# Kernel optimization log

Measured on AMD Instinct MI355X. Metric: run time of the kernel, lower is better.

Reference implementation:

```python
import jax, jax.numpy as jnp
import numpy as np

HEADS = 8
NEG_SLOPE = 0.2  # PyG GATConv default LeakyReLU slope


def _gat_layer(x, src, dst, W, a_src, a_dst, bias, heads, out_ch):
    """PyG-style GATConv (concat heads, self-loops already appended, eval mode).
    x: [N, F_in]; src/dst: [E_tot] int; W: [F_in, heads*out_ch];
    a_src/a_dst: [heads, out_ch]; bias: [heads*out_ch].
    """
    N = x.shape[0]
    h = (x @ W).reshape(N, heads, out_ch)                      # [N, H, C]
    # per-node attention logits (gathered per edge as scalars, not features)
    al_s = jnp.einsum('nhc,hc->nh', h, a_src)                  # [N, H]
    al_d = jnp.einsum('nhc,hc->nh', h, a_dst)                  # [N, H]
    e = jax.nn.leaky_relu(al_s[src] + al_d[dst], negative_slope=NEG_SLOPE)  # [E, H]
    # segment softmax over incoming edges of each target node (stable)
    e_max = jax.ops.segment_max(e, dst, num_segments=N)        # self-loops => no empty segments
    ex = jnp.exp(e - e_max[dst])
    denom = jax.ops.segment_sum(ex, dst, num_segments=N)
    alpha = ex / (denom[dst] + 1e-16)                          # [E, H]
    # gather source features, weight, scatter-add to targets
    out = jax.ops.segment_sum(h[src] * alpha[:, :, None], dst, num_segments=N)  # [N, H, C]
    return out.reshape(N, heads * out_ch) + bias


def setup_inputs() -> dict:
    key = jax.random.key(0)
    ks = jax.random.split(key, 16)
    N, E, F_IN, NUM_CLASSES = 50000, 1600000, 128, 16
    s = 0.1
    return {
        'x': jax.random.normal(ks[0], (N, F_IN), dtype=jnp.float32),
        'edge_index': jax.random.randint(ks[1], (2, E), 0, N, dtype=jnp.int64),
        # GAT layer 1: 128 -> 8 heads x 8
        'W1': jax.random.normal(ks[2], (F_IN, 64), dtype=jnp.float32) * s,
        'a1_src': jax.random.normal(ks[3], (8, 8), dtype=jnp.float32) * s,
        'a1_dst': jax.random.normal(ks[4], (8, 8), dtype=jnp.float32) * s,
        'b1': jnp.zeros((64,), dtype=jnp.float32),
        # GAT layer 2: 64 -> 8 heads x 4
        'W2': jax.random.normal(ks[5], (64, 32), dtype=jnp.float32) * s,
        'a2_src': jax.random.normal(ks[6], (8, 4), dtype=jnp.float32) * s,
        'a2_dst': jax.random.normal(ks[7], (8, 4), dtype=jnp.float32) * s,
        'b2': jnp.zeros((32,), dtype=jnp.float32),
        # torch MultiheadAttention(32, 8): packed in_proj [96,32], out_proj [32,32]
        'in_proj_w': jax.random.normal(ks[8], (96, 32), dtype=jnp.float32) * s,
        'in_proj_b': jnp.zeros((96,), dtype=jnp.float32),
        'out_proj_w': jax.random.normal(ks[9], (32, 32), dtype=jnp.float32) * s,
        'out_proj_b': jnp.zeros((32,), dtype=jnp.float32),
        # fc: 32 -> num_classes
        'fc_w': jax.random.normal(ks[10], (NUM_CLASSES, 32), dtype=jnp.float32) * s,
        'fc_b': jnp.zeros((NUM_CLASSES,), dtype=jnp.float32),
    }


def reference(x, edge_index, W1, a1_src, a1_dst, b1, W2, a2_src, a2_dst, b2,
              in_proj_w, in_proj_b, out_proj_w, out_proj_b, fc_w, fc_b):
    N = x.shape[0]
    loops = jnp.arange(N, dtype=edge_index.dtype)
    src = jnp.concatenate([edge_index[0], loops])  # PyG add_self_loops=True
    dst = jnp.concatenate([edge_index[1], loops])

    h = jax.nn.elu(_gat_layer(x, src, dst, W1, a1_src, a1_dst, b1, HEADS, 8))   # [N, 64]
    h = jax.nn.elu(_gat_layer(h, src, dst, W2, a2_src, a2_dst, b2, HEADS, 4))   # [N, 32]

    # MultiheadAttention on h.unsqueeze(0): shape [1, N, 32] with torch's
    # seq-first layout => seq_len = 1, batch = N. Softmax over a single key
    # is identically 1 for every head, so out = out_proj(v_proj(h)).
    v = h @ in_proj_w[64:96].T + in_proj_b[64:96]   # v-projection slice of packed in_proj
    h = v @ out_proj_w.T + out_proj_b               # [N, 32]

    logits = h @ fc_w.T + fc_b                      # [N, num_classes]
    return jax.nn.log_softmax(logits, axis=1)
```

## Files before the change

### kernel.cpp

```cpp
#include <hip/hip_runtime.h>
#include <hip/hip_bf16.h>
#include <math.h>


#define BSHIFT 7
#define BMASK  ((1 << BSHIFT) - 1)
#define MAXNB  512
#define TILE   8192
#define XST    136

typedef __attribute__((ext_vector_type(8))) short short8;
typedef __attribute__((ext_vector_type(4))) float floatx4;
typedef __attribute__((ext_vector_type(2))) float floatx2;

__device__ __forceinline__ unsigned short f2bf(float f) {
    union { float f; unsigned int u; } v; v.f = f;
    unsigned int u = v.u;
    return (unsigned short)((u + 0x7FFFu + ((u >> 16) & 1u)) >> 16);
}
__device__ __forceinline__ float lrelu(float e) { return fmaxf(e, 0.2f * e); }
__device__ __forceinline__ float elu(float o) {
    return (o > 0.f) ? o : (__expf(o) - 1.f);
}

__global__ __launch_bounds__(256) void bin_scatter1_kernel(
    const int* __restrict__ ei, int E, int Et, int NB, int CAP,
    int* __restrict__ gcount, unsigned int* __restrict__ rec) {
    __shared__ unsigned int lrec[TILE];
    __shared__ int h[MAXNB];
    __shared__ int cur[MAXNB];
    int t = threadIdx.x;
    for (int i = t; i < NB; i += 256) h[i] = 0;
    int tile0 = blockIdx.x * TILE;
    int cnt = Et - tile0; if (cnt > TILE) cnt = TILE;
    __syncthreads();
    for (int j = t; j < cnt; j += 256) {
        int jj = tile0 + j;
        int srcv, d;
        if (jj < E) { srcv = ei[jj]; d = ei[E + jj]; } else { srcv = jj - E; d = jj - E; }
        lrec[j] = (unsigned)srcv | ((unsigned)d << 16);
        atomicAdd(&h[d >> BSHIFT], 1);
    }
    __syncthreads();
    for (int i = t; i < NB; i += 256)
        cur[i] = h[i] ? atomicAdd(&gcount[i], h[i]) : 0;
    __syncthreads();
    for (int j = t; j < cnt; j += 256) {
        unsigned v = lrec[j];
        int b = v >> (16 + BSHIFT);
        int pos = atomicAdd(&cur[b], 1);
        if (pos < CAP)
            rec[(size_t)b * CAP + pos] =
                (v & 0xFFFFu) | ((((v >> 16) & BMASK)) << 16);
    }
}

__global__ __launch_bounds__(512) void scan_fold_kernel(
    const int* __restrict__ gcount, int* __restrict__ bbase, int NB, int CAP,
    const float* __restrict__ in_proj_w, const float* __restrict__ in_proj_b,
    const float* __restrict__ out_proj_w, const float* __restrict__ out_proj_b,
    const float* __restrict__ fc_w, const float* __restrict__ fc_b,
    float* __restrict__ M, float* __restrict__ bf) {
    __shared__ int s[512];
    __shared__ float Wvo[32 * 32];
    __shared__ float bvo[32];
    int t = threadIdx.x;
    if (blockIdx.x == 0) {
        int v = 0;
        if (t < NB) { v = gcount[t]; if (v > CAP) v = CAP; }
        s[t] = v;
        __syncthreads();
        for (int off = 1; off < 512; off <<= 1) {
            int u = (t >= off) ? s[t - off] : 0;
            __syncthreads();
            s[t] += u;
            __syncthreads();
        }
        if (t < NB) bbase[t] = s[t] - v;
    } else {
        const float* Wv = in_proj_w + 64 * 32;
        const float* bv = in_proj_b + 64;
        for (int idx = t; idx < 1024; idx += 512) {
            int i = idx >> 5, j = idx & 31;
            float acc = 0.f;
            for (int k = 0; k < 32; ++k) acc += out_proj_w[i * 32 + k] * Wv[k * 32 + j];
            Wvo[idx] = acc;
        }
        if (t < 32) {
            float acc = 0.f;
            for (int k = 0; k < 32; ++k) acc += out_proj_w[t * 32 + k] * bv[k];
            bvo[t] = acc + out_proj_b[t];
        }
        __syncthreads();
        for (int idx = t; idx < 16 * 32; idx += 512) {
            int cc = idx >> 5, j = idx & 31;
            float acc = 0.f;
            for (int i = 0; i < 32; ++i) acc += fc_w[cc * 32 + i] * Wvo[i * 32 + j];
            M[idx] = acc;
        }
        if (t < 16) {
            float acc = 0.f;
            for (int i = 0; i < 32; ++i) acc += fc_w[t * 32 + i] * bvo[i];
            bf[t] = acc + fc_b[t];
        }
    }
}

__global__ __launch_bounds__(256) void csr_finalize_kernel(
    const unsigned int* __restrict__ rec, const int* __restrict__ gcount,
    const int* __restrict__ bbase, int* __restrict__ rowp,
    unsigned short* __restrict__ esrc, int N, int Et, int CAP) {
    __shared__ int h[128];
    __shared__ int nb[128];
    __shared__ int cur[128];
    int b = blockIdx.x, t = threadIdx.x;
    size_t rbase = (size_t)b * CAP;
    int cnt = gcount[b]; if (cnt > CAP) cnt = CAP;
    int obase = bbase[b];
    if (t < 128) h[t] = 0;
    __syncthreads();
    for (int i = t; i < cnt; i += 256)
        atomicAdd(&h[(rec[rbase + i] >> 16) & 127], 1);
    __syncthreads();
    if (t == 0) {
        int run = obase;
        for (int i = 0; i < 128; ++i) { nb[i] = run; run += h[i]; }
    }
    __syncthreads();
    if (t < 128) cur[t] = nb[t];
    int n0 = b << BSHIFT;
    if (t < 128 && n0 + t < N) rowp[n0 + t] = nb[t];
    if (b == 0 && t == 0) rowp[N] = Et;
    __syncthreads();
    for (int i = t; i < cnt; i += 256) {
        unsigned r = rec[rbase + i];
        int pos = atomicAdd(&cur[(r >> 16) & 127], 1);
        esrc[pos] = (unsigned short)(r & 0xFFFFu);
    }
}

__global__ __launch_bounds__(256) void gemm1_mfma_kernel(
    const float* __restrict__ x, const float* __restrict__ W,
    const float* __restrict__ a_src, const float* __restrict__ a_dst,
    unsigned int* __restrict__ h1p, float* __restrict__ als,
    float* __restrict__ ald, int N) {
    __shared__ __align__(16) unsigned short xs[64 * XST];
    __shared__ __align__(16) unsigned short wt[64 * XST];
    int t = threadIdx.x;
    int nb = blockIdx.x * 64;
#pragma unroll
    for (int r = 0; r < 8; ++r) {
        int p = t + 256 * r;
        int row = p >> 5;
        int c4  = p & 31;
        int n = nb + row;
        float4 v = (n < N) ? ((const float4*)x)[(size_t)n * 32 + c4]
                           : make_float4(0.f, 0.f, 0.f, 0.f);
        unsigned short* dst = &xs[row * XST + c4 * 4];
        dst[0] = f2bf(v.x); dst[1] = f2bf(v.y);
        dst[2] = f2bf(v.z); dst[3] = f2bf(v.w);
    }
    {
        int n = t & 63, kg = t >> 6;
#pragma unroll
        for (int c = 0; c < 4; ++c) {
            int k0 = kg * 32 + c * 8;
            unsigned short* dst = &wt[n * XST + k0];
#pragma unroll
            for (int j = 0; j < 8; ++j)
                dst[j] = f2bf(W[(k0 + j) * 64 + n]);
        }
    }
    __syncthreads();
    int wave = t >> 6, lane = t & 63;
    int m16 = lane & 15, quad = lane >> 4;
    floatx4 acc[4];
#pragma unroll
    for (int i = 0; i < 4; ++i) acc[i] = (floatx4){0.f, 0.f, 0.f, 0.f};
#pragma unroll
    for (int k = 0; k < 4; ++k) {
        int koff = k * 32 + quad * 8;
        short8 afrag = *(const short8*)&xs[(wave * 16 + m16) * XST + koff];
#pragma unroll
        for (int nt = 0; nt < 4; ++nt) {
            short8 bfrag = *(const short8*)&wt[(nt * 16 + m16) * XST + koff];
            acc[nt] = __builtin_amdgcn_mfma_f32_16x16x32_bf16(afrag, bfrag, acc[nt], 0, 0, 0);
        }
    }
    __syncthreads();
    float* hs = (float*)xs;
#pragma unroll
    for (int nt = 0; nt < 4; ++nt)
#pragma unroll
        for (int r = 0; r < 4; ++r)
            hs[(wave * 16 + quad * 4 + r) * 65 + nt * 16 + m16] = acc[nt][r];
    __syncthreads();
    float asv = a_src[lane], adv = a_dst[lane];
    for (int itn = 0; itn < 16; ++itn) {
        int nl = wave * 16 + itn;
        int n = nb + nl;
        if (n >= N) break;
        float v = hs[nl * 65 + lane];
        float ps = v * asv, pd = v * adv;
        ps += __shfl_xor(ps, 1); ps += __shfl_xor(ps, 2); ps += __shfl_xor(ps, 4);
        pd += __shfl_xor(pd, 1); pd += __shfl_xor(pd, 2); pd += __shfl_xor(pd, 4);
        if ((lane & 7) == 0) {
            als[n * 8 + (lane >> 3)] = ps;
            ald[n * 8 + (lane >> 3)] = pd;
        }
        if (lane < 16) {
            const float* hr = &hs[nl * 65 + lane * 4];
            int pk = __builtin_amdgcn_cvt_pk_fp8_f32(hr[0], hr[1], 0, false);
            pk = __builtin_amdgcn_cvt_pk_fp8_f32(hr[2], hr[3], pk, true);
            h1p[(size_t)n * 16 + lane] = (unsigned)pk;
        }
    }
}

__global__ __launch_bounds__(256) void gat_agg64_g2_kernel(
    const int* __restrict__ rowp, const unsigned short* __restrict__ esrc,
    const unsigned int* __restrict__ feat, const float* __restrict__ als,
    const float* __restrict__ ald_arr, const float* __restrict__ bias,
    const float* __restrict__ W2, const float* __restrict__ a2s,
    const float* __restrict__ a2d,
    char* __restrict__ rec2, float* __restrict__ ald2, int N) {
    __shared__ __align__(16) float W2p[2][8][32][4];
    __shared__ __align__(16) float oL[4][64];
    __shared__ __align__(16) float h2L[4][32];
    int t = threadIdx.x;
    for (int idx = t; idx < 2048; idx += 256) {
        int k = idx >> 5, l = idx & 31;
        W2p[k >> 5][(k & 31) >> 2][l][k & 3] = W2[idx];
    }
    __syncthreads();
    const int lane = t & 63;
    const int wv = t >> 6;
    const int e = lane >> 4;
    const int c = lane & 15;
    const int hd = c >> 1;
    int n = blockIdx.x * 4 + wv;
    if (n >= N) return;
    float aldv = ald_arr[n * 8 + hd];
    int beg = rowp[n], end = rowp[n + 1];
    float dA = 0.f, dB = 0.f;
    floatx2 p0a = {0.f, 0.f}, p0b = {0.f, 0.f};
    floatx2 p1a = {0.f, 0.f}, p1b = {0.f, 0.f};
    floatx2 p2a = {0.f, 0.f}, p2b = {0.f, 0.f};
    floatx2 p3a = {0.f, 0.f}, p3b = {0.f, 0.f};
    int i = beg;
    for (; i + 32 <= end; i += 32) {
        int s0 = esrc[i + e],      s1 = esrc[i + 4 + e];
        int s2 = esrc[i + 8 + e],  s3 = esrc[i + 12 + e];
        int s4 = esrc[i + 16 + e], s5 = esrc[i + 20 + e];
        int s6 = esrc[i + 24 + e], s7 = esrc[i + 28 + e];
        float e0 = als[s0 * 8 + hd], e1 = als[s1 * 8 + hd];
        float e2 = als[s2 * 8 + hd], e3 = als[s3 * 8 + hd];
        float e4 = als[s4 * 8 + hd], e5 = als[s5 * 8 + hd];
        float e6 = als[s6 * 8 + hd], e7 = als[s7 * 8 + hd];
        unsigned g0 = feat[s0 * 16 + c], g1 = feat[s1 * 16 + c];
        unsigned g2 = feat[s2 * 16 + c], g3 = feat[s3 * 16 + c];
        unsigned g4 = feat[s4 * 16 + c], g5 = feat[s5 * 16 + c];
        unsigned g6 = feat[s6 * 16 + c], g7 = feat[s7 * 16 + c];
        float w0 = __expf(lrelu(e0 + aldv));
        float w1 = __expf(lrelu(e1 + aldv));
        float w2 = __expf(lrelu(e2 + aldv));
        float w3 = __expf(lrelu(e3 + aldv));
        float w4 = __expf(lrelu(e4 + aldv));
        float w5 = __expf(lrelu(e5 + aldv));
        float w6 = __expf(lrelu(e6 + aldv));
        float w7 = __expf(lrelu(e7 + aldv));
        dA += w0 + w2; dB += w1 + w3;
        dA += w4 + w6; dB += w5 + w7;
        p0a += w0 * __builtin_amdgcn_cvt_pk_f32_fp8(g0, false);
        p0b += w0 * __builtin_amdgcn_cvt_pk_f32_fp8(g0, true);
        p1a += w1 * __builtin_amdgcn_cvt_pk_f32_fp8(g1, false);
        p1b += w1 * __builtin_amdgcn_cvt_pk_f32_fp8(g1, true);
        p2a += w2 * __builtin_amdgcn_cvt_pk_f32_fp8(g2, false);
        p2b += w2 * __builtin_amdgcn_cvt_pk_f32_fp8(g2, true);
        p3a += w3 * __builtin_amdgcn_cvt_pk_f32_fp8(g3, false);
        p3b += w3 * __builtin_amdgcn_cvt_pk_f32_fp8(g3, true);
        p0a += w4 * __builtin_amdgcn_cvt_pk_f32_fp8(g4, false);
        p0b += w4 * __builtin_amdgcn_cvt_pk_f32_fp8(g4, true);
        p1a += w5 * __builtin_amdgcn_cvt_pk_f32_fp8(g5, false);
        p1b += w5 * __builtin_amdgcn_cvt_pk_f32_fp8(g5, true);
        p2a += w6 * __builtin_amdgcn_cvt_pk_f32_fp8(g6, false);
        p2b += w6 * __builtin_amdgcn_cvt_pk_f32_fp8(g6, true);
        p3a += w7 * __builtin_amdgcn_cvt_pk_f32_fp8(g7, false);
        p3b += w7 * __builtin_amdgcn_cvt_pk_f32_fp8(g7, true);
    }
    for (; i < end; i += 16) {
        int i0 = i + e, i1 = i + 4 + e, i2 = i + 8 + e, i3 = i + 12 + e;
        bool v0 = i0 < end, v1 = i1 < end, v2 = i2 < end, v3 = i3 < end;
        int c0 = v0 ? i0 : beg;
        int c1 = v1 ? i1 : beg;
        int c2 = v2 ? i2 : beg;
        int c3 = v3 ? i3 : beg;
        int s0 = esrc[c0], s1 = esrc[c1], s2 = esrc[c2], s3 = esrc[c3];
        float e0 = als[s0 * 8 + hd], e1 = als[s1 * 8 + hd];
        float e2 = als[s2 * 8 + hd], e3 = als[s3 * 8 + hd];
        unsigned g0 = feat[s0 * 16 + c], g1 = feat[s1 * 16 + c];
        unsigned g2 = feat[s2 * 16 + c], g3 = feat[s3 * 16 + c];
        float w0 = v0 ? __expf(lrelu(e0 + aldv)) : 0.f;
        float w1 = v1 ? __expf(lrelu(e1 + aldv)) : 0.f;
        float w2 = v2 ? __expf(lrelu(e2 + aldv)) : 0.f;
        float w3 = v3 ? __expf(lrelu(e3 + aldv)) : 0.f;
        dA += w0 + w2; dB += w1 + w3;
        p0a += w0 * __builtin_amdgcn_cvt_pk_f32_fp8(g0, false);
        p0b += w0 * __builtin_amdgcn_cvt_pk_f32_fp8(g0, true);
        p1a += w1 * __builtin_amdgcn_cvt_pk_f32_fp8(g1, false);
        p1b += w1 * __builtin_amdgcn_cvt_pk_f32_fp8(g1, true);
        p2a += w2 * __builtin_amdgcn_cvt_pk_f32_fp8(g2, false);
        p2b += w2 * __builtin_amdgcn_cvt_pk_f32_fp8(g2, true);
        p3a += w3 * __builtin_amdgcn_cvt_pk_f32_fp8(g3, false);
        p3b += w3 * __builtin_amdgcn_cvt_pk_f32_fp8(g3, true);
    }
    float d = dA + dB;
    floatx2 Pa = (p0a + p1a) + (p2a + p3a);
    floatx2 Pb = (p0b + p1b) + (p2b + p3b);
    float P0 = Pa.x, P1 = Pa.y, P2 = Pb.x, P3 = Pb.y;
    d  += __shfl_xor(d, 16);  d  += __shfl_xor(d, 32);
    P0 += __shfl_xor(P0, 16); P0 += __shfl_xor(P0, 32);
    P1 += __shfl_xor(P1, 16); P1 += __shfl_xor(P1, 32);
    P2 += __shfl_xor(P2, 16); P2 += __shfl_xor(P2, 32);
    P3 += __shfl_xor(P3, 16); P3 += __shfl_xor(P3, 32);
    float inv = 1.f / (d + 1e-16f);
    float4 bv = ((const float4*)bias)[c];
    float o0 = elu(P0 * inv + bv.x);
    float o1 = elu(P1 * inv + bv.y);
    float o2 = elu(P2 * inv + bv.z);
    float o3 = elu(P3 * inv + bv.w);
    if (lane < 16) *(float4*)&oL[wv][c * 4] = make_float4(o0, o1, o2, o3);
    const int l = lane & 31, kh = lane >> 5;
    const float* orow = &oL[wv][kh * 32];
    float a0 = 0.f, a1 = 0.f, a2 = 0.f, a3 = 0.f;
#pragma unroll
    for (int g = 0; g < 8; ++g) {
        float4 ov = *(const float4*)&orow[g * 4];
        float4 wv4 = *(const float4*)&W2p[kh][g][l][0];
        a0 += ov.x * wv4.x; a1 += ov.y * wv4.y;
        a2 += ov.z * wv4.z; a3 += ov.w * wv4.w;
    }
    float acc = (a0 + a1) + (a2 + a3);
    acc += __shfl_xor(acc, 32);
    float ps = acc * a2s[l], pd = acc * a2d[l];
    ps += __shfl_xor(ps, 1); ps += __shfl_xor(ps, 2);
    pd += __shfl_xor(pd, 1); pd += __shfl_xor(pd, 2);
    if (lane < 32) {
        h2L[wv][l] = acc;
        if ((l & 3) == 0) {
            *(float*)(rec2 + (size_t)n * 64 + 4 * (l >> 2)) = ps;
            ald2[n * 8 + (l >> 2)] = pd;
        }
    }
    if (lane < 8) {
        const float* hr = &h2L[wv][lane * 4];
        int pk = __builtin_amdgcn_cvt_pk_fp8_f32(hr[0], hr[1], 0, false);
        pk = __builtin_amdgcn_cvt_pk_fp8_f32(hr[2], hr[3], pk, true);
        *(unsigned*)(rec2 + (size_t)n * 64 + 32 + 4 * lane) = (unsigned)pk;
    }
}

__global__ __launch_bounds__(256) void gat_agg32_fin_kernel(
    const int* __restrict__ rowp, const unsigned short* __restrict__ esrc,
    const char* __restrict__ rec2, const float* __restrict__ ald_arr,
    const float* __restrict__ bias,
    const float* __restrict__ M, const float* __restrict__ bf,
    float* __restrict__ out, int N) {
    __shared__ __align__(16) float Mp[8][16][4];
    __shared__ float bfs[16];
    __shared__ __align__(16) float oL[4][32];
    int t = threadIdx.x;
    for (int i = t; i < 512; i += 256) {
        int j = i >> 5, k = i & 31;
        Mp[k >> 2][j][k & 3] = M[i];
    }
    if (t < 16) bfs[t] = bf[t];
    __syncthreads();
    const int lane = t & 63;
    const int wv = t >> 6;
    const int e = lane >> 3;
    const int c = lane & 7;
    const int aoff = 4 * c;
    const int foff = 32 + 4 * c;
    int n = blockIdx.x * 4 + wv;
    if (n >= N) return;
    float aldv = ald_arr[n * 8 + c];
    int beg = rowp[n], end = rowp[n + 1];
    float d0 = 0.f, d1 = 0.f, d2 = 0.f, d3 = 0.f;
    floatx2 p0a = {0.f, 0.f}, p0b = {0.f, 0.f};
    floatx2 p1a = {0.f, 0.f}, p1b = {0.f, 0.f};
    floatx2 p2a = {0.f, 0.f}, p2b = {0.f, 0.f};
    floatx2 p3a = {0.f, 0.f}, p3b = {0.f, 0.f};
    int base = beg;
    for (; base + 32 <= end; base += 32) {
        int s0 = esrc[base + e],      s1 = esrc[base + 8 + e];
        int s2 = esrc[base + 16 + e], s3 = esrc[base + 24 + e];
        const char* r0 = rec2 + (size_t)s0 * 64;
        const char* r1 = rec2 + (size_t)s1 * 64;
        const char* r2 = rec2 + (size_t)s2 * 64;
        const char* r3 = rec2 + (size_t)s3 * 64;
        float e0 = *(const float*)(r0 + aoff) + aldv;
        float e1 = *(const float*)(r1 + aoff) + aldv;
        float e2 = *(const float*)(r2 + aoff) + aldv;
        float e3 = *(const float*)(r3 + aoff) + aldv;
        unsigned g0 = *(const unsigned*)(r0 + foff);
        unsigned g1 = *(const unsigned*)(r1 + foff);
        unsigned g2 = *(const unsigned*)(r2 + foff);
        unsigned g3 = *(const unsigned*)(r3 + foff);
        float w0 = __expf(lrelu(e0));
        float w1 = __expf(lrelu(e1));
        float w2 = __expf(lrelu(e2));
        float w3 = __expf(lrelu(e3));
        d0 += w0; d1 += w1; d2 += w2; d3 += w3;
        p0a += w0 * __builtin_amdgcn_cvt_pk_f32_fp8(g0, false);
        p0b += w0 * __builtin_amdgcn_cvt_pk_f32_fp8(g0, true);
        p1a += w1 * __builtin_amdgcn_cvt_pk_f32_fp8(g1, false);
        p1b += w1 * __builtin_amdgcn_cvt_pk_f32_fp8(g1, true);
        p2a += w2 * __builtin_amdgcn_cvt_pk_f32_fp8(g2, false);
        p2b += w2 * __builtin_amdgcn_cvt_pk_f32_fp8(g2, true);
        p3a += w3 * __builtin_amdgcn_cvt_pk_f32_fp8(g3, false);
        p3b += w3 * __builtin_amdgcn_cvt_pk_f32_fp8(g3, true);
    }
    for (; base < end; base += 32) {
        int i0 = base + e;
        int i1 = base + 8 + e;
        int i2 = base + 16 + e;
        int i3 = base + 24 + e;
        bool v0 = i0 < end, v1 = i1 < end, v2 = i2 < end, v3 = i3 < end;
        int c0 = v0 ? i0 : beg;
        int c1 = v1 ? i1 : beg;
        int c2 = v2 ? i2 : beg;
        int c3 = v3 ? i3 : beg;
        int s0 = esrc[c0], s1 = esrc[c1], s2 = esrc[c2], s3 = esrc[c3];
        const char* r0 = rec2 + (size_t)s0 * 64;
        const char* r1 = rec2 + (size_t)s1 * 64;
        const char* r2 = rec2 + (size_t)s2 * 64;
        const char* r3 = rec2 + (size_t)s3 * 64;
        float e0 = *(const float*)(r0 + aoff) + aldv;
        float e1 = *(const float*)(r1 + aoff) + aldv;
        float e2 = *(const float*)(r2 + aoff) + aldv;
        float e3 = *(const float*)(r3 + aoff) + aldv;
        unsigned g0 = *(const unsigned*)(r0 + foff);
        unsigned g1 = *(const unsigned*)(r1 + foff);
        unsigned g2 = *(const unsigned*)(r2 + foff);
        unsigned g3 = *(const unsigned*)(r3 + foff);
        float w0 = v0 ? __expf(lrelu(e0)) : 0.f;
        float w1 = v1 ? __expf(lrelu(e1)) : 0.f;
        float w2 = v2 ? __expf(lrelu(e2)) : 0.f;
        float w3 = v3 ? __expf(lrelu(e3)) : 0.f;
        d0 += w0; d1 += w1; d2 += w2; d3 += w3;
        p0a += w0 * __builtin_amdgcn_cvt_pk_f32_fp8(g0, false);
        p0b += w0 * __builtin_amdgcn_cvt_pk_f32_fp8(g0, true);
        p1a += w1 * __builtin_amdgcn_cvt_pk_f32_fp8(g1, false);
        p1b += w1 * __builtin_amdgcn_cvt_pk_f32_fp8(g1, true);
        p2a += w2 * __builtin_amdgcn_cvt_pk_f32_fp8(g2, false);
        p2b += w2 * __builtin_amdgcn_cvt_pk_f32_fp8(g2, true);
        p3a += w3 * __builtin_amdgcn_cvt_pk_f32_fp8(g3, false);
        p3b += w3 * __builtin_amdgcn_cvt_pk_f32_fp8(g3, true);
    }
    float d = (d0 + d1) + (d2 + d3);
    floatx2 Pa = (p0a + p1a) + (p2a + p3a);
    floatx2 Pb = (p0b + p1b) + (p2b + p3b);
    float P0 = Pa.x, P1 = Pa.y, P2 = Pb.x, P3 = Pb.y;
    d  += __shfl_xor(d, 8);  d  += __shfl_xor(d, 16);  d  += __shfl_xor(d, 32);
    P0 += __shfl_xor(P0, 8); P0 += __shfl_xor(P0, 16); P0 += __shfl_xor(P0, 32);
    P1 += __shfl_xor(P1, 8); P1 += __shfl_xor(P1, 16); P1 += __shfl_xor(P1, 32);
    P2 += __shfl_xor(P2, 8); P2 += __shfl_xor(P2, 16); P2 += __shfl_xor(P2, 32);
    P3 += __shfl_xor(P3, 8); P3 += __shfl_xor(P3, 16); P3 += __shfl_xor(P3, 32);
    float inv = 1.f / (d + 1e-16f);
    float4 bv = ((const float4*)bias)[c];
    float o0 = elu(P0 * inv + bv.x);
    float o1 = elu(P1 * inv + bv.y);
    float o2 = elu(P2 * inv + bv.z);
    float o3 = elu(P3 * inv + bv.w);
    if (lane < 8) *(float4*)&oL[wv][c * 4] = make_float4(o0, o1, o2, o3);
    const int j = lane & 15;
    const float* orow = oL[wv];
    float a0 = 0.f, a1 = 0.f, a2 = 0.f, a3 = 0.f;
#pragma unroll
    for (int g = 0; g < 8; ++g) {
        float4 ov = *(const float4*)&orow[g * 4];
        float4 mv = *(const float4*)&Mp[g][j][0];
        a0 += ov.x * mv.x; a1 += ov.y * mv.y;
        a2 += ov.z * mv.z; a3 += ov.w * mv.w;
    }
    float logit = (a0 + a1) + (a2 + a3) + bfs[j];
    float mx = logit;
    mx = fmaxf(mx, __shfl_xor(mx, 1));
    mx = fmaxf(mx, __shfl_xor(mx, 2));
    mx = fmaxf(mx, __shfl_xor(mx, 4));
    mx = fmaxf(mx, __shfl_xor(mx, 8));
    float ex = __expf(logit - mx);
    float se = ex;
    se += __shfl_xor(se, 1);
    se += __shfl_xor(se, 2);
    se += __shfl_xor(se, 4);
    se += __shfl_xor(se, 8);
    float res = logit - (mx + __logf(se));
    if (lane < 16) out[(size_t)n * 16 + j] = res;
}

extern "C" void kernel_launch(void* const* d_in, const int* in_sizes, int n_in,
                              void* d_out, int out_size, void* d_ws, size_t ws_size,
                              hipStream_t stream) {
    const float* x   = (const float*)d_in[0];
    const int*   ei  = (const int*)d_in[1];
    const float* W1  = (const float*)d_in[2];
    const float* a1s = (const float*)d_in[3];
    const float* a1d = (const float*)d_in[4];
    const float* b1  = (const float*)d_in[5];
    const float* W2  = (const float*)d_in[6];
    const float* a2s = (const float*)d_in[7];
    const float* a2d = (const float*)d_in[8];
    const float* b2  = (const float*)d_in[9];
    const float* ipw = (const float*)d_in[10];
    const float* ipb = (const float*)d_in[11];
    const float* opw = (const float*)d_in[12];
    const float* opb = (const float*)d_in[13];
    const float* fcw = (const float*)d_in[14];
    const float* fcb = (const float*)d_in[15];
    float* out = (float*)d_out;

    int N = in_sizes[0] / 128;
    int E = in_sizes[1] / 2;
    int Et = E + N;
    int NB = (N + BMASK) >> BSHIFT;
    int NTILES = (Et + TILE - 1) / TILE;
    int CAP = Et / NB;
    CAP = CAP + CAP / 8 + 256;
    CAP = (CAP + 255) & ~255;

    char* ws = (char*)d_ws;
    size_t off = 0;
    auto alloc = [&](size_t bytes) -> void* {
        void* p = ws + off;
        off += bytes;
        off = (off + 255) & ~(size_t)255;
        return p;
    };
    int*   bcount = (int*)alloc(MAXNB * 4);
    int*   bbase  = (int*)alloc(MAXNB * 4);
    unsigned int*   rec  = (unsigned int*)alloc((size_t)NB * CAP * 4);
    int*   rowp   = (int*)alloc((size_t)(N + 1) * 4);
    unsigned short* esrc = (unsigned short*)alloc((size_t)Et * 2);
    unsigned int* h1p = (unsigned int*)alloc((size_t)N * 16 * 4);
    float* al1s  = (float*)alloc((size_t)N * 8 * 4);
    float* al1d  = (float*)alloc((size_t)N * 8 * 4);
    char* rec2   = (char*)alloc((size_t)N * 64);
    float* al2d  = (float*)alloc((size_t)N * 8 * 4);
    float* Mf    = (float*)alloc(512 * 4);
    float* bff   = (float*)alloc(16 * 4);
    (void)ws_size; (void)n_in; (void)out_size;

    hipMemsetAsync(bcount, 0, MAXNB * 4, stream);
    bin_scatter1_kernel<<<NTILES, 256, 0, stream>>>(ei, E, Et, NB, CAP, bcount, rec);
    scan_fold_kernel<<<2, 512, 0, stream>>>(bcount, bbase, NB, CAP,
                                            ipw, ipb, opw, opb, fcw, fcb, Mf, bff);
    csr_finalize_kernel<<<NB, 256, 0, stream>>>(rec, bcount, bbase, rowp, esrc, N, Et, CAP);

    gemm1_mfma_kernel<<<(N + 63) / 64, 256, 0, stream>>>(x, W1, a1s, a1d, h1p, al1s, al1d, N);
    gat_agg64_g2_kernel<<<(N + 3) / 4, 256, 0, stream>>>(
        rowp, esrc, h1p, al1s, al1d, b1, W2, a2s, a2d, rec2, al2d, N);
    gat_agg32_fin_kernel<<<(N + 3) / 4, 256, 0, stream>>>(
        rowp, esrc, rec2, al2d, b2, Mf, bff, out, N);
}
```

Baseline: 230.7 us.

## Fuse GEMM1, edge binning and weight folding into one launch; pack per-node records

Merges the first-layer MFMA GEMM, the edge bin-scatter and the output-weight folding into a single kernel whose blocks are partitioned by role. The separate scan kernel is dropped, and each CSR-finalize block now computes its own bucket base by reducing the preceding bucket counts. Source attention logits and fp8 features are packed into one 128-byte per-node record, so the layer-1 aggregation's gather touches one line per source instead of two arrays. This saves launches and gather traffic, at the cost of redundant prefix reductions and a shared-memory footprint sized for the largest role.

Measured after the change: 211.9 us. 1.09x faster.

```diff
diff --git a/kernel.cpp b/kernel.cpp
--- a/kernel.cpp
+++ b/kernel.cpp
@@ -8,6 +8,7 @@
 #define MAXNB  512
 #define TILE   8192
 #define XST    136
+#define SMBYTES 36864
 
 typedef __attribute__((ext_vector_type(8))) short short8;
 typedef __attribute__((ext_vector_type(4))) float floatx4;
@@ -23,64 +24,123 @@
     return (o > 0.f) ? o : (__expf(o) - 1.f);
 }
 
-__global__ __launch_bounds__(256) void bin_scatter1_kernel(
+__global__ __launch_bounds__(256) void fused_pre_kernel(
+    const float* __restrict__ x, const float* __restrict__ W,
+    const float* __restrict__ a_src, const float* __restrict__ a_dst,
+    char* __restrict__ rec1, float* __restrict__ ald, int N, int GB,
     const int* __restrict__ ei, int E, int Et, int NB, int CAP,
-    int* __restrict__ gcount, unsigned int* __restrict__ rec) {
-    __shared__ unsigned int lrec[TILE];
-    __shared__ int h[MAXNB];
-    __shared__ int cur[MAXNB];
-    int t = threadIdx.x;
-    for (int i = t; i < NB; i += 256) h[i] = 0;
-    int tile0 = blockIdx.x * TILE;
-    int cnt = Et - tile0; if (cnt > TILE) cnt = TILE;
-    __syncthreads();
-    for (int j = t; j < cnt; j += 256) {
-        int jj = tile0 + j;
-        int srcv, d;
-        if (jj < E) { srcv = ei[jj]; d = ei[E + jj]; } else { srcv = jj - E; d = jj - E; }
-        lrec[j] = (unsigned)srcv | ((unsigned)d << 16);
-        atomicAdd(&h[d >> BSHIFT], 1);
-    }
-    __syncthreads();
-    for (int i = t; i < NB; i += 256)
-        cur[i] = h[i] ? atomicAdd(&gcount[i], h[i]) : 0;
-    __syncthreads();
-    for (int j = t; j < cnt; j += 256) {
-        unsigned v = lrec[j];
-        int b = v >> (16 + BSHIFT);
-        int pos = atomicAdd(&cur[b], 1);
-        if (pos < CAP)
-            rec[(size_t)b * CAP + pos] =
-                (v & 0xFFFFu) | ((((v >> 16) & BMASK)) << 16);
-    }
-}
-
-__global__ __launch_bounds__(512) void scan_fold_kernel(
-    const int* __restrict__ gcount, int* __restrict__ bbase, int NB, int CAP,
+    int* __restrict__ gcount, unsigned int* __restrict__ rec, int NT,
     const float* __restrict__ in_proj_w, const float* __restrict__ in_proj_b,
     const float* __restrict__ out_proj_w, const float* __restrict__ out_proj_b,
     const float* __restrict__ fc_w, const float* __restrict__ fc_b,
     float* __restrict__ M, float* __restrict__ bf) {
-    __shared__ int s[512];
-    __shared__ float Wvo[32 * 32];
-    __shared__ float bvo[32];
+    __shared__ __align__(16) char sm[SMBYTES];
     int t = threadIdx.x;
-    if (blockIdx.x == 0) {
-        int v = 0;
-        if (t < NB) { v = gcount[t]; if (v > CAP) v = CAP; }
-        s[t] = v;
-        __syncthreads();
-        for (int off = 1; off < 512; off <<= 1) {
-            int u = (t >= off) ? s[t - off] : 0;
-            __syncthreads();
-            s[t] += u;
-            __syncthreads();
-        }
-        if (t < NB) bbase[t] = s[t] - v;
+    int bid = blockIdx.x;
+    if (bid < GB) {
+        unsigned short* xs = (unsigned short*)sm;
+        unsigned short* wt = xs + 64 * XST;
+        int nb = bid * 64;
+#pragma unroll
+        for (int r = 0; r < 8; ++r) {
+            int p = t + 256 * r;
+            int row = p >> 5;
+            int c4  = p & 31;
+            int n = nb + row;
+            float4 v = (n < N) ? ((const float4*)x)[(size_t)n * 32 + c4]
+                               : make_float4(0.f, 0.f, 0.f, 0.f);
+            unsigned short* dst = &xs[row * XST + c4 * 4];
+            dst[0] = f2bf(v.x); dst[1] = f2bf(v.y);
+            dst[2] = f2bf(v.z); dst[3] = f2bf(v.w);
+        }
+        {
+            int n = t & 63, kg = t >> 6;
+#pragma unroll
+            for (int c = 0; c < 4; ++c) {
+                int k0 = kg * 32 + c * 8;
+                unsigned short* dst = &wt[n * XST + k0];
+#pragma unroll
+                for (int j = 0; j < 8; ++j)
+                    dst[j] = f2bf(W[(k0 + j) * 64 + n]);
+            }
+        }
+        __syncthreads();
+        int wave = t >> 6, lane = t & 63;
+        int m16 = lane & 15, quad = lane >> 4;
+        floatx4 acc[4];
+#pragma unroll
+        for (int i = 0; i < 4; ++i) acc[i] = (floatx4){0.f, 0.f, 0.f, 0.f};
+#pragma unroll
+        for (int k = 0; k < 4; ++k) {
+            int koff = k * 32 + quad * 8;
+            short8 afrag = *(const short8*)&xs[(wave * 16 + m16) * XST + koff];
+#pragma unroll
+            for (int nt = 0; nt < 4; ++nt) {
+                short8 bfrag = *(const short8*)&wt[(nt * 16 + m16) * XST + koff];
+                acc[nt] = __builtin_amdgcn_mfma_f32_16x16x32_bf16(afrag, bfrag, acc[nt], 0, 0, 0);
+            }
+        }
+        __syncthreads();
+        float* hs = (float*)sm;
+#pragma unroll
+        for (int nt = 0; nt < 4; ++nt)
+#pragma unroll
+            for (int r = 0; r < 4; ++r)
+                hs[(wave * 16 + quad * 4 + r) * 65 + nt * 16 + m16] = acc[nt][r];
+        __syncthreads();
+        float asv = a_src[lane], adv = a_dst[lane];
+        for (int itn = 0; itn < 16; ++itn) {
+            int nl = wave * 16 + itn;
+            int n = nb + nl;
+            if (n >= N) break;
+            float v = hs[nl * 65 + lane];
+            float ps = v * asv, pd = v * adv;
+            ps += __shfl_xor(ps, 1); ps += __shfl_xor(ps, 2); ps += __shfl_xor(ps, 4);
+            pd += __shfl_xor(pd, 1); pd += __shfl_xor(pd, 2); pd += __shfl_xor(pd, 4);
+            if ((lane & 7) == 0) {
+                *(float*)(rec1 + (size_t)n * 128 + 4 * (lane >> 3)) = ps;
+                ald[n * 8 + (lane >> 3)] = pd;
+            }
+            if (lane < 16) {
+                const float* hr = &hs[nl * 65 + lane * 4];
+                int pk = __builtin_amdgcn_cvt_pk_fp8_f32(hr[0], hr[1], 0, false);
+                pk = __builtin_amdgcn_cvt_pk_fp8_f32(hr[2], hr[3], pk, true);
+                *(unsigned*)(rec1 + (size_t)n * 128 + 64 + 4 * lane) = (unsigned)pk;
+            }
+        }
+    } else if (bid < GB + NT) {
+        unsigned int* lrec = (unsigned int*)sm;
+        int* h   = (int*)(sm + TILE * 4);
+        int* cur = (int*)(sm + TILE * 4 + MAXNB * 4);
+        for (int i = t; i < NB; i += 256) h[i] = 0;
+        int tile0 = (bid - GB) * TILE;
+        int cnt = Et - tile0; if (cnt > TILE) cnt = TILE;
+        __syncthreads();
+        for (int j = t; j < cnt; j += 256) {
+            int jj = tile0 + j;
+            int srcv, d;
+            if (jj < E) { srcv = ei[jj]; d = ei[E + jj]; } else { srcv = jj - E; d = jj - E; }
+            lrec[j] = (unsigned)srcv | ((unsigned)d << 16);
+            atomicAdd(&h[d >> BSHIFT], 1);
+        }
+        __syncthreads();
+        for (int i = t; i < NB; i += 256)
+            cur[i] = h[i] ? atomicAdd(&gcount[i], h[i]) : 0;
+        __syncthreads();
+        for (int j = t; j < cnt; j += 256) {
+            unsigned v = lrec[j];
+            int b = v >> (16 + BSHIFT);
+            int pos = atomicAdd(&cur[b], 1);
+            if (pos < CAP)
+                rec[(size_t)b * CAP + pos] =
+                    (v & 0xFFFFu) | ((((v >> 16) & BMASK)) << 16);
+        }
     } else {
+        float* Wvo = (float*)sm;
+        float* bvo = (float*)(sm + 4096);
         const float* Wv = in_proj_w + 64 * 32;
         const float* bv = in_proj_b + 64;
-        for (int idx = t; idx < 1024; idx += 512) {
+        for (int idx = t; idx < 1024; idx += 256) {
             int i = idx >> 5, j = idx & 31;
             float acc = 0.f;
             for (int k = 0; k < 32; ++k) acc += out_proj_w[i * 32 + k] * Wv[k * 32 + j];
@@ -92,7 +152,7 @@
             bvo[t] = acc + out_proj_b[t];
         }
         __syncthreads();
-        for (int idx = t; idx < 16 * 32; idx += 512) {
+        for (int idx = t; idx < 16 * 32; idx += 256) {
             int cc = idx >> 5, j = idx & 31;
             float acc = 0.f;
             for (int i = 0; i < 32; ++i) acc += fc_w[cc * 32 + i] * Wvo[i * 32 + j];
@@ -108,17 +168,28 @@
 
 __global__ __launch_bounds__(256) void csr_finalize_kernel(
     const unsigned int* __restrict__ rec, const int* __restrict__ gcount,
-    const int* __restrict__ bbase, int* __restrict__ rowp,
-    unsigned short* __restrict__ esrc, int N, int Et, int CAP) {
+    int* __restrict__ rowp, unsigned short* __restrict__ esrc,
+    int N, int Et, int CAP) {
     __shared__ int h[128];
     __shared__ int nb[128];
     __shared__ int cur[128];
+    __shared__ int ssum[256];
     int b = blockIdx.x, t = threadIdx.x;
     size_t rbase = (size_t)b * CAP;
     int cnt = gcount[b]; if (cnt > CAP) cnt = CAP;
-    int obase = bbase[b];
     if (t < 128) h[t] = 0;
+    int acc = 0;
+    for (int i = t; i < b; i += 256) {
+        int v = gcount[i];
+        acc += (v < CAP) ? v : CAP;
+    }
+    ssum[t] = acc;
     __syncthreads();
+    for (int off = 128; off >= 1; off >>= 1) {
+        if (t < off) ssum[t] += ssum[t + off];
+        __syncthreads();
+    }
+    int obase = ssum[0];
     for (int i = t; i < cnt; i += 256)
         atomicAdd(&h[(rec[rbase + i] >> 16) & 127], 1);
     __syncthreads();
@@ -139,88 +210,10 @@
     }
 }
 
-__global__ __launch_bounds__(256) void gemm1_mfma_kernel(
-    const float* __restrict__ x, const float* __restrict__ W,
-    const float* __restrict__ a_src, const float* __restrict__ a_dst,
-    unsigned int* __restrict__ h1p, float* __restrict__ als,
-    float* __restrict__ ald, int N) {
-    __shared__ __align__(16) unsigned short xs[64 * XST];
-    __shared__ __align__(16) unsigned short wt[64 * XST];
-    int t = threadIdx.x;
-    int nb = blockIdx.x * 64;
-#pragma unroll
-    for (int r = 0; r < 8; ++r) {
-        int p = t + 256 * r;
-        int row = p >> 5;
-        int c4  = p & 31;
-        int n = nb + row;
-        float4 v = (n < N) ? ((const float4*)x)[(size_t)n * 32 + c4]
-                           : make_float4(0.f, 0.f, 0.f, 0.f);
-        unsigned short* dst = &xs[row * XST + c4 * 4];
-        dst[0] = f2bf(v.x); dst[1] = f2bf(v.y);
-        dst[2] = f2bf(v.z); dst[3] = f2bf(v.w);
-    }
-    {
-        int n = t & 63, kg = t >> 6;
-#pragma unroll
-        for (int c = 0; c < 4; ++c) {
-            int k0 = kg * 32 + c * 8;
-            unsigned short* dst = &wt[n * XST + k0];
-#pragma unroll
-            for (int j = 0; j < 8; ++j)
-                dst[j] = f2bf(W[(k0 + j) * 64 + n]);
-        }
-    }
-    __syncthreads();
-    int wave = t >> 6, lane = t & 63;
-    int m16 = lane & 15, quad = lane >> 4;
-    floatx4 acc[4];
-#pragma unroll
-    for (int i = 0; i < 4; ++i) acc[i] = (floatx4){0.f, 0.f, 0.f, 0.f};
-#pragma unroll
-    for (int k = 0; k < 4; ++k) {
-        int koff = k * 32 + quad * 8;
-        short8 afrag = *(const short8*)&xs[(wave * 16 + m16) * XST + koff];
-#pragma unroll
-        for (int nt = 0; nt < 4; ++nt) {
-            short8 bfrag = *(const short8*)&wt[(nt * 16 + m16) * XST + koff];
-            acc[nt] = __builtin_amdgcn_mfma_f32_16x16x32_bf16(afrag, bfrag, acc[nt], 0, 0, 0);
-        }
-    }
-    __syncthreads();
-    float* hs = (float*)xs;
-#pragma unroll
-    for (int nt = 0; nt < 4; ++nt)
-#pragma unroll
-        for (int r = 0; r < 4; ++r)
-            hs[(wave * 16 + quad * 4 + r) * 65 + nt * 16 + m16] = acc[nt][r];
-    __syncthreads();
-    float asv = a_src[lane], adv = a_dst[lane];
-    for (int itn = 0; itn < 16; ++itn) {
-        int nl = wave * 16 + itn;
-        int n = nb + nl;
-        if (n >= N) break;
-        float v = hs[nl * 65 + lane];
-        float ps = v * asv, pd = v * adv;
-        ps += __shfl_xor(ps, 1); ps += __shfl_xor(ps, 2); ps += __shfl_xor(ps, 4);
-        pd += __shfl_xor(pd, 1); pd += __shfl_xor(pd, 2); pd += __shfl_xor(pd, 4);
-        if ((lane & 7) == 0) {
-            als[n * 8 + (lane >> 3)] = ps;
-            ald[n * 8 + (lane >> 3)] = pd;
-        }
-        if (lane < 16) {
-            const float* hr = &hs[nl * 65 + lane * 4];
-            int pk = __builtin_amdgcn_cvt_pk_fp8_f32(hr[0], hr[1], 0, false);
-            pk = __builtin_amdgcn_cvt_pk_fp8_f32(hr[2], hr[3], pk, true);
-            h1p[(size_t)n * 16 + lane] = (unsigned)pk;
-        }
-    }
-}
-
 __global__ __launch_bounds__(256) void gat_agg64_g2_kernel(
     const int* __restrict__ rowp, const unsigned short* __restrict__ esrc,
-    const unsigned int* __restrict__ feat, const float* __restrict__ als,
-    const float* __restrict__ ald_arr, const float* __restrict__ bias,
+    const char* __restrict__ rec1, const float* __restrict__ ald_arr,
+    const float* __restrict__ bias,
     const float* __restrict__ W2, const float* __restrict__ a2s,
     const float* __restrict__ a2d,
     char* __restrict__ rec2, float* __restrict__ ald2, int N) {
@@ -238,6 +231,8 @@
     const int e = lane >> 4;
     const int c = lane & 15;
     const int hd = c >> 1;
+    const int aoff = 4 * hd;
+    const int foff = 64 + 4 * c;
     int n = blockIdx.x * 4 + wv;
     if (n >= N) return;
     float aldv = ald_arr[n * 8 + hd];
@@ -253,14 +248,22 @@
         int s2 = esrc[i + 8 + e],  s3 = esrc[i + 12 + e];
         int s4 = esrc[i + 16 + e], s5 = esrc[i + 20 + e];
         int s6 = esrc[i + 24 + e], s7 = esrc[i + 28 + e];
-        float e0 = als[s0 * 8 + hd], e1 = als[s1 * 8 + hd];
-        float e2 = als[s2 * 8 + hd], e3 = als[s3 * 8 + hd];
-        float e4 = als[s4 * 8 + hd], e5 = als[s5 * 8 + hd];
-        float e6 = als[s6 * 8 + hd], e7 = als[s7 * 8 + hd];
-        unsigned g0 = feat[s0 * 16 + c], g1 = feat[s1 * 16 + c];
-        unsigned g2 = feat[s2 * 16 + c], g3 = feat[s3 * 16 + c];
-        unsigned g4 = feat[s4 * 16 + c], g5 = feat[s5 * 16 + c];
-        unsigned g6 = feat[s6 * 16 + c], g7 = feat[s7 * 16 + c];
+        const char* r0 = rec1 + (size_t)s0 * 128;
+        const char* r1 = rec1 + (size_t)s1 * 128;
+        const char* r2 = rec1 + (size_t)s2 * 128;
+        const char* r3 = rec1 + (size_t)s3 * 128;
+        const char* r4 = rec1 + (size_t)s4 * 128;
+        const char* r5 = rec1 + (size_t)s5 * 128;
+        const char* r6 = rec1 + (size_t)s6 * 128;
+        const char* r7 = rec1 + (size_t)s7 * 128;
+        float e0 = *(const float*)(r0 + aoff), e1 = *(const float*)(r1 + aoff);
+        float e2 = *(const float*)(r2 + aoff), e3 = *(const float*)(r3 + aoff);
+        float e4 = *(const float*)(r4 + aoff), e5 = *(const float*)(r5 + aoff);
+        float e6 = *(const float*)(r6 + aoff), e7 = *(const float*)(r7 + aoff);
+        unsigned g0 = *(const unsigned*)(r0 + foff), g1 = *(const unsigned*)(r1 + foff);
+        unsigned g2 = *(const unsigned*)(r2 + foff), g3 = *(const unsigned*)(r3 + foff);
+        unsigned g4 = *(const unsigned*)(r4 + foff), g5 = *(const unsigned*)(r5 + foff);
+        unsigned g6 = *(const unsigned*)(r6 + foff), g7 = *(const unsigned*)(r7 + foff);
         float w0 = __expf(lrelu(e0 + aldv));
         float w1 = __expf(lrelu(e1 + aldv));
         float w2 = __expf(lrelu(e2 + aldv));
@@ -296,10 +299,14 @@
         int c2 = v2 ? i2 : beg;
         int c3 = v3 ? i3 : beg;
         int s0 = esrc[c0], s1 = esrc[c1], s2 = esrc[c2], s3 = esrc[c3];
-        float e0 = als[s0 * 8 + hd], e1 = als[s1 * 8 + hd];
-        float e2 = als[s2 * 8 + hd], e3 = als[s3 * 8 + hd];
-        unsigned g0 = feat[s0 * 16 + c], g1 = feat[s1 * 16 + c];
-        unsigned g2 = feat[s2 * 16 + c], g3 = feat[s3 * 16 + c];
+        const char* r0 = rec1 + (size_t)s0 * 128;
+        const char* r1 = rec1 + (size_t)s1 * 128;
+        const char* r2 = rec1 + (size_t)s2 * 128;
+        const char* r3 = rec1 + (size_t)s3 * 128;
+        float e0 = *(const float*)(r0 + aoff), e1 = *(const float*)(r1 + aoff);
+        float e2 = *(const float*)(r2 + aoff), e3 = *(const float*)(r3 + aoff);
+        unsigned g0 = *(const unsigned*)(r0 + foff), g1 = *(const unsigned*)(r1 + foff);
+        unsigned g2 = *(const unsigned*)(r2 + foff), g3 = *(const unsigned*)(r3 + foff);
         float w0 = v0 ? __expf(lrelu(e0 + aldv)) : 0.f;
         float w1 = v1 ? __expf(lrelu(e1 + aldv)) : 0.f;
         float w2 = v2 ? __expf(lrelu(e2 + aldv)) : 0.f;
@@ -526,6 +533,7 @@
     int Et = E + N;
     int NB = (N + BMASK) >> BSHIFT;
     int NTILES = (Et + TILE - 1) / TILE;
+    int GB = (N + 63) / 64;
     int CAP = Et / NB;
     CAP = CAP + CAP / 8 + 256;
     CAP = (CAP + 255) & ~255;
@@ -539,12 +547,10 @@
         return p;
     };
     int*   bcount = (int*)alloc(MAXNB * 4);
-    int*   bbase  = (int*)alloc(MAXNB * 4);
     unsigned int*   rec  = (unsigned int*)alloc((size_t)NB * CAP * 4);
     int*   rowp   = (int*)alloc((size_t)(N + 1) * 4);
     unsigned short* esrc = (unsigned short*)alloc((size_t)Et * 2);
-    unsigned int* h1p = (unsigned int*)alloc((size_t)N * 16 * 4);
-    float* al1s  = (float*)alloc((size_t)N * 8 * 4);
+    char* rec1   = (char*)alloc((size_t)N * 128);
     float* al1d  = (float*)alloc((size_t)N * 8 * 4);
     char* rec2   = (char*)alloc((size_t)N * 64);
     float* al2d  = (float*)alloc((size_t)N * 8 * 4);
@@ -553,14 +559,14 @@
     (void)ws_size; (void)n_in; (void)out_size;
 
     hipMemsetAsync(bcount, 0, MAXNB * 4, stream);
-    bin_scatter1_kernel<<<NTILES, 256, 0, stream>>>(ei, E, Et, NB, CAP, bcount, rec);
-    scan_fold_kernel<<<2, 512, 0, stream>>>(bcount, bbase, NB, CAP,
-                                            ipw, ipb, opw, opb, fcw, fcb, Mf, bff);
-    csr_finalize_kernel<<<NB, 256, 0, stream>>>(rec, bcount, bbase, rowp, esrc, N, Et, CAP);
-
-    gemm1_mfma_kernel<<<(N + 63) / 64, 256, 0, stream>>>(x, W1, a1s, a1d, h1p, al1s, al1d, N);
+    fused_pre_kernel<<<GB + NTILES + 1, 256, 0, stream>>>(
+        x, W1, a1s, a1d, rec1, al1d, N, GB,
+        ei, E, Et, NB, CAP, bcount, rec, NTILES,
+        ipw, ipb, opw, opb, fcw, fcb, Mf, bff);
+    csr_finalize_kernel<<<NB, 256, 0, stream>>>(rec, bcount, rowp, esrc, N, Et, CAP);
+
     gat_agg64_g2_kernel<<<(N + 3) / 4, 256, 0, stream>>>(
-        rowp, esrc, h1p, al1s, al1d, b1, W2, a2s, a2d, rec2, al2d, N);
+        rowp, esrc, rec1, al1d, b1, W2, a2s, a2d, rec2, al2d, N);
     gat_agg32_fin_kernel<<<(N + 3) / 4, 256, 0, stream>>>(
         rowp, esrc, rec2, al2d, b2, Mf, bff, out, N);
 }
```
